# Performance work log

Hardware: AMD Instinct MI355X
Metric: run time of the kernel (lower is better)

The kernel has to match this reference:

```python
import jax, jax.numpy as jnp
import numpy as np

H, I, E, K = 1024, 2048, 8, 2
B, T = 4, 2048


def setup_inputs() -> dict:
    key = jax.random.key(0)
    k0, k1, k2, k3 = jax.random.split(key, 4)
    x = jax.random.normal(k0, (B, T, H), dtype=jnp.float32)
    Wg = jax.random.normal(k1, (E, H), dtype=jnp.float32) * 0.02   # gate: Linear(H->E), weight [E,H]
    W1 = jax.random.normal(k2, (E, I, H), dtype=jnp.float32) * 0.02  # per-expert fc1 weights [I,H]
    W2 = jax.random.normal(k3, (E, H, I), dtype=jnp.float32) * 0.02  # per-expert fc2 weights [H,I]
    return {"x": x, "Wg": Wg, "W1": W1, "W2": W2, "top_k": K}


def reference(x, Wg, W1, W2, top_k):
    b, t, h = x.shape
    xf = x.reshape(-1, h)                                  # [N,H], N=B*T
    gate_probs = jax.nn.softmax(xf @ Wg.T, axis=-1)        # [N,E]
    topk_vals, topk_idx = jax.lax.top_k(gate_probs, top_k) # [N,k]
    # Dense all-expert SiLU-MLP (faithful to the original dense MoE):
    hid = jax.nn.silu(jnp.einsum('nh,eih->nei', xf, W1))   # [N,E,I]
    all_outs = jnp.einsum('nei,ehi->neh', hid, W2)         # [N,E,H]
    topk_outs = jnp.take_along_axis(all_outs, topk_idx[:, :, None], axis=1)  # [N,k,H]
    weighted = (topk_outs * topk_vals[:, :, None]).sum(axis=1)               # [N,H]
    return weighted.reshape(b, t, h)
```

## Files before the change

### kernel.cpp

```cpp
#include <hip/hip_runtime.h>
#include <hip/hip_bf16.h>

#define HH 1024
#define II 2048
#define EE 8
#define NTOK 8192
#define NPAIR (NTOK * 2)

typedef __attribute__((ext_vector_type(8))) short bf16x8;
typedef __attribute__((ext_vector_type(4))) float f32x4;
typedef unsigned int u32;

__device__ __forceinline__ ushort f2bf(float f) {
    union { float f; unsigned u; } v; v.f = f;
    unsigned r = v.u + 0x7fffu + ((v.u >> 16) & 1u);
    return (ushort)(r >> 16);
}

__device__ __forceinline__ void gload16(const void* g, void* l) {
    __builtin_amdgcn_global_load_lds((const __attribute__((address_space(1))) u32*)g,
                                     (__attribute__((address_space(3))) u32*)l, 16, 0, 0);
}

__device__ __forceinline__ int expert_off(const int* __restrict__ counts, int e) {
    int off = 0;
#pragma unroll
    for (int i = 0; i < EE; i++) off += (i < e) ? counts[i] : 0;
    return off;
}

__global__ __launch_bounds__(256) void cvtw_kernel(
    const float* __restrict__ W1, const float* __restrict__ W2,
    ushort* __restrict__ W1b, ushort* __restrict__ W2b)
{
    const int N1 = EE * II * HH / 4;
    const int i = blockIdx.x * 256 + threadIdx.x;
    const float4 f = (i < N1) ? ((const float4*)W1)[i] : ((const float4*)W2)[i - N1];
    union { ushort h[4]; uint2 u; } pk;
    pk.h[0] = f2bf(f.x); pk.h[1] = f2bf(f.y); pk.h[2] = f2bf(f.z); pk.h[3] = f2bf(f.w);
    if (i < N1) ((uint2*)W1b)[i] = pk.u;
    else        ((uint2*)W2b)[i - N1] = pk.u;
}

__global__ __launch_bounds__(256) void gate_kernel(
    const float* __restrict__ x, const float* __restrict__ Wg,
    int* __restrict__ counts, int* __restrict__ tki, float* __restrict__ tkv,
    ushort* __restrict__ xb)
{
    __shared__ int hist[EE];
    const int tid = threadIdx.x;
    if (tid < EE) hist[tid] = 0;
    __syncthreads();

    const int w = tid >> 6, lane = tid & 63;

#pragma unroll 1
    for (int t = 0; t < 8; t++) {
        const int n = blockIdx.x * 32 + w * 8 + t;
        const float* xr = x + (size_t)n * HH;
        float4 xv[4];
#pragma unroll
        for (int c = 0; c < 4; c++) xv[c] = *(const float4*)(xr + c * 256 + lane * 4);

#pragma unroll
        for (int c = 0; c < 4; c++) {
            union { ushort h[4]; uint2 u; } pk;
            pk.h[0] = f2bf(xv[c].x); pk.h[1] = f2bf(xv[c].y);
            pk.h[2] = f2bf(xv[c].z); pk.h[3] = f2bf(xv[c].w);
            *(uint2*)(xb + (size_t)n * HH + c * 256 + lane * 4) = pk.u;
        }

        float dot[EE];
#pragma unroll
        for (int e = 0; e < EE; e++) {
            float s = 0.f;
#pragma unroll
            for (int c = 0; c < 4; c++) {
                const float4 wv = *(const float4*)(Wg + e * HH + c * 256 + lane * 4);
                s += xv[c].x * wv.x + xv[c].y * wv.y + xv[c].z * wv.z + xv[c].w * wv.w;
            }
            for (int off = 32; off > 0; off >>= 1) s += __shfl_down(s, off);
            dot[e] = s;
        }
        if (lane == 0) {
            float m = dot[0];
#pragma unroll
            for (int e = 1; e < EE; e++) m = fmaxf(m, dot[e]);
            float p[EE]; float sum = 0.f;
#pragma unroll
            for (int e = 0; e < EE; e++) { p[e] = __expf(dot[e] - m); sum += p[e]; }
            const float inv = 1.f / sum;
            int i0 = 0; float v0 = p[0];
#pragma unroll
            for (int e = 1; e < EE; e++) if (p[e] > v0) { v0 = p[e]; i0 = e; }
            int i1 = -1; float v1 = -1.f;
#pragma unroll
            for (int e = 0; e < EE; e++) if (e != i0 && p[e] > v1) { v1 = p[e]; i1 = e; }
            tki[n * 2 + 0] = i0; tkv[n * 2 + 0] = v0 * inv;
            tki[n * 2 + 1] = i1; tkv[n * 2 + 1] = v1 * inv;
            atomicAdd(&hist[i0], 1);
            atomicAdd(&hist[i1], 1);
        }
    }
    __syncthreads();
    if (tid < EE) atomicAdd(&counts[tid], hist[tid]);
}

__global__ __launch_bounds__(256) void scatter_kernel(
    const int* __restrict__ tki, const float* __restrict__ tkv,
    const int* __restrict__ counts,
    int* __restrict__ cursor, int* __restrict__ stok, float* __restrict__ sval)
{
    __shared__ int hist[EE];
    __shared__ int base[EE];
    const int tid = threadIdx.x;
    const int id = blockIdx.x * 256 + tid;
    if (tid < EE) hist[tid] = 0;
    __syncthreads();
    const int e = tki[id];
    const int loc = atomicAdd(&hist[e], 1);
    __syncthreads();
    if (tid < EE) {
        int off = 0;
        for (int i = 0; i < tid; i++) off += counts[i];
        base[tid] = off + atomicAdd(&cursor[tid], hist[tid]);
    }
    __syncthreads();
    const int p = base[e] + loc;
    stok[p] = id >> 1;
    sval[p] = tkv[id];
}

template <bool PRE>
__global__ __launch_bounds__(256) void fc1_kernel(
    const float* __restrict__ x, const ushort* __restrict__ xb,
    const float* __restrict__ W1, const ushort* __restrict__ W1b,
    const int* __restrict__ counts,
    const int* __restrict__ stok, ushort* __restrict__ hid)
{
    const int e = blockIdx.z;
    const int cnt = counts[e];
    const int row0 = blockIdx.y * 128;
    if (row0 >= cnt) return;
    const int off = expert_off(counts, e);
    const int col0 = blockIdx.x * 128;

    __shared__ __align__(16) ushort As[128 * 64];
    __shared__ __align__(16) ushort Bs[128 * 64];

    const int tid = threadIdx.x;
    const int w = tid >> 6, lane = tid & 63;
    const int quad = lane >> 4, l16 = lane & 15;
    const int wm = (w >> 1) * 64, wn = (w & 1) * 64;
    const int l7 = l16 & 7;

    f32x4 acc[4][4];
#pragma unroll
    for (int mi = 0; mi < 4; mi++)
#pragma unroll
        for (int ni = 0; ni < 4; ni++) acc[mi][ni] = f32x4{0.f, 0.f, 0.f, 0.f};

    const int sub = lane >> 3;
    const int chk = lane & 7;
    const int gchk = chk ^ sub;
    int tokA[4];
    const int fr = tid >> 1;
    const int fc = (tid & 1) * 32;
    int tokF = 0;
    if (PRE) {
#pragma unroll
        for (int i = 0; i < 4; i++) {
            int r = row0 + (w * 4 + i) * 8 + sub;
            if (r >= cnt) r = cnt - 1;
            tokA[i] = stok[off + r];
        }
    } else {
        int r = row0 + fr;
        if (r >= cnt) r = cnt - 1;
        tokF = stok[off + r];
    }

    if (PRE) {
#pragma unroll 1
        for (int it = 0; it < HH / 64; it++) {
            const int k0 = it * 64;
            __syncthreads();
#pragma unroll
            for (int i = 0; i < 4; i++) {
                const ushort* gA = xb + (size_t)tokA[i] * HH + k0 + gchk * 8;
                gload16(gA, &As[(w * 4 + i) * 512]);
                const ushort* gB = W1b + ((size_t)e * II + col0 + (w * 4 + i) * 8 + sub) * HH + k0 + gchk * 8;
                gload16(gB, &Bs[(w * 4 + i) * 512]);
            }
            __syncthreads();
#pragma unroll
            for (int kk = 0; kk < 2; kk++) {
                const int pos = ((kk * 4 + quad) ^ l7) * 8;
                bf16x8 af[4], bb[4];
#pragma unroll
                for (int mi = 0; mi < 4; mi++)
                    af[mi] = *(const bf16x8*)&As[(wm + mi * 16 + l16) * 64 + pos];
#pragma unroll
                for (int ni = 0; ni < 4; ni++)
                    bb[ni] = *(const bf16x8*)&Bs[(wn + ni * 16 + l16) * 64 + pos];
#pragma unroll
                for (int mi = 0; mi < 4; mi++)
#pragma unroll
                    for (int ni = 0; ni < 4; ni++)
                        acc[mi][ni] = __builtin_amdgcn_mfma_f32_16x16x32_bf16(af[mi], bb[ni], acc[mi][ni], 0, 0, 0);
            }
        }
    } else {
#pragma unroll 1
        for (int k0 = 0; k0 < HH; k0 += 64) {
            __syncthreads();
#pragma unroll
            for (int c = 0; c < 32; c += 4) {
                const int u = fc + c;
                const int sw = ((u >> 3) ^ (fr & 7)) * 8 + (u & 7);
                const float4 f = *(const float4*)(x + (size_t)tokF * HH + k0 + u);
                union { ushort h[4]; uint2 u2; } pk;
                pk.h[0] = f2bf(f.x); pk.h[1] = f2bf(f.y); pk.h[2] = f2bf(f.z); pk.h[3] = f2bf(f.w);
                *(uint2*)&As[fr * 64 + sw] = pk.u2;
                const float4 g = *(const float4*)(W1 + ((size_t)e * II + col0 + fr) * HH + k0 + u);
                pk.h[0] = f2bf(g.x); pk.h[1] = f2bf(g.y); pk.h[2] = f2bf(g.z); pk.h[3] = f2bf(g.w);
                *(uint2*)&Bs[fr * 64 + sw] = pk.u2;
            }
            __syncthreads();
#pragma unroll
            for (int kk = 0; kk < 2; kk++) {
                const int pos = ((kk * 4 + quad) ^ l7) * 8;
                bf16x8 af[4], bb[4];
#pragma unroll
                for (int mi = 0; mi < 4; mi++)
                    af[mi] = *(const bf16x8*)&As[(wm + mi * 16 + l16) * 64 + pos];
#pragma unroll
                for (int ni = 0; ni < 4; ni++)
                    bb[ni] = *(const bf16x8*)&Bs[(wn + ni * 16 + l16) * 64 + pos];
#pragma unroll
                for (int mi = 0; mi < 4; mi++)
#pragma unroll
                    for (int ni = 0; ni < 4; ni++)
                        acc[mi][ni] = __builtin_amdgcn_mfma_f32_16x16x32_bf16(af[mi], bb[ni], acc[mi][ni], 0, 0, 0);
            }
        }
    }

    const int cnt_rem = cnt - row0;
#pragma unroll
    for (int mi = 0; mi < 4; mi++) {
#pragma unroll
        for (int j = 0; j < 4; j++) {
            const int r = wm + mi * 16 + quad * 4 + j;
            if (r < cnt_rem) {
                ushort* hrow = hid + (size_t)(off + row0 + r) * II + col0 + wn + l16;
#pragma unroll
                for (int ni = 0; ni < 4; ni++) {
                    const float v = acc[mi][ni][j];
                    const float s = v / (1.f + __expf(-v));
                    hrow[ni * 16] = f2bf(s);
                }
            }
        }
    }
}

template <bool PRE>
__global__ __launch_bounds__(256) void fc2_kernel(
    const ushort* __restrict__ hid,
    const float* __restrict__ W2, const ushort* __restrict__ W2b,
    const int* __restrict__ counts,
    const int* __restrict__ stok, const float* __restrict__ sval,
    float* __restrict__ out)
{
    const int e = blockIdx.z;
    const int cnt = counts[e];
    const int row0 = blockIdx.y * 128;
    if (row0 >= cnt) return;
    const int off = expert_off(counts, e);
    const int col0 = blockIdx.x * 128;

    __shared__ __align__(16) ushort As[128 * 64];
    __shared__ __align__(16) ushort Bs[128 * 64];

    const int tid = threadIdx.x;
    const int w = tid >> 6, lane = tid & 63;
    const int quad = lane >> 4, l16 = lane & 15;
    const int wm = (w >> 1) * 64, wn = (w & 1) * 64;
    const int l7 = l16 & 7;

    f32x4 acc[4][4];
#pragma unroll
    for (int mi = 0; mi < 4; mi++)
#pragma unroll
        for (int ni = 0; ni < 4; ni++) acc[mi][ni] = f32x4{0.f, 0.f, 0.f, 0.f};

    const int sub = lane >> 3;
    const int chk = lane & 7;
    const int gchk = chk ^ sub;
    size_t slotA[4];
#pragma unroll
    for (int i = 0; i < 4; i++) {
        int s = off + row0 + (w * 4 + i) * 8 + sub;
        if (s > NPAIR - 1) s = NPAIR - 1;
        slotA[i] = (size_t)s;
    }
    const int fr = tid >> 1;
    const int fc = (tid & 1) * 32;

    if (PRE) {
#pragma unroll 1
        for (int it = 0; it < II / 64; it++) {
            const int k0 = it * 64;
            __syncthreads();
#pragma unroll
            for (int i = 0; i < 4; i++) {
                const ushort* gA = hid + slotA[i] * II + k0 + gchk * 8;
                gload16(gA, &As[(w * 4 + i) * 512]);
                const ushort* gB = W2b + ((size_t)e * HH + col0 + (w * 4 + i) * 8 + sub) * II + k0 + gchk * 8;
                gload16(gB, &Bs[(w * 4 + i) * 512]);
            }
            __syncthreads();
#pragma unroll
            for (int kk = 0; kk < 2; kk++) {
                const int pos = ((kk * 4 + quad) ^ l7) * 8;
                bf16x8 af[4], bb[4];
#pragma unroll
                for (int mi = 0; mi < 4; mi++)
                    af[mi] = *(const bf16x8*)&As[(wm + mi * 16 + l16) * 64 + pos];
#pragma unroll
                for (int ni = 0; ni < 4; ni++)
                    bb[ni] = *(const bf16x8*)&Bs[(wn + ni * 16 + l16) * 64 + pos];
#pragma unroll
                for (int mi = 0; mi < 4; mi++)
#pragma unroll
                    for (int ni = 0; ni < 4; ni++)
                        acc[mi][ni] = __builtin_amdgcn_mfma_f32_16x16x32_bf16(af[mi], bb[ni], acc[mi][ni], 0, 0, 0);
            }
        }
    } else {
#pragma unroll 1
        for (int k0 = 0; k0 < II; k0 += 64) {
            __syncthreads();
#pragma unroll
            for (int i = 0; i < 4; i++) {
                const ushort* gA = hid + slotA[i] * II + k0 + gchk * 8;
                gload16(gA, &As[(w * 4 + i) * 512]);
            }
#pragma unroll
            for (int c = 0; c < 32; c += 4) {
                const int u = fc + c;
                const int sw = ((u >> 3) ^ (fr & 7)) * 8 + (u & 7);
                const float4 g = *(const float4*)(W2 + ((size_t)e * HH + col0 + fr) * II + k0 + u);
                union { ushort h[4]; uint2 u2; } pk;
                pk.h[0] = f2bf(g.x); pk.h[1] = f2bf(g.y); pk.h[2] = f2bf(g.z); pk.h[3] = f2bf(g.w);
                *(uint2*)&Bs[fr * 64 + sw] = pk.u2;
            }
            __syncthreads();
#pragma unroll
            for (int kk = 0; kk < 2; kk++) {
                const int pos = ((kk * 4 + quad) ^ l7) * 8;
                bf16x8 af[4], bb[4];
#pragma unroll
                for (int mi = 0; mi < 4; mi++)
                    af[mi] = *(const bf16x8*)&As[(wm + mi * 16 + l16) * 64 + pos];
#pragma unroll
                for (int ni = 0; ni < 4; ni++)
                    bb[ni] = *(const bf16x8*)&Bs[(wn + ni * 16 + l16) * 64 + pos];
#pragma unroll
                for (int mi = 0; mi < 4; mi++)
#pragma unroll
                    for (int ni = 0; ni < 4; ni++)
                        acc[mi][ni] = __builtin_amdgcn_mfma_f32_16x16x32_bf16(af[mi], bb[ni], acc[mi][ni], 0, 0, 0);
            }
        }
    }

    const int cnt_rem = cnt - row0;
#pragma unroll
    for (int mi = 0; mi < 4; mi++) {
#pragma unroll
        for (int j = 0; j < 4; j++) {
            const int r = wm + mi * 16 + quad * 4 + j;
            if (r < cnt_rem) {
                const int p = off + row0 + r;
                const int token = stok[p];
                const float val = sval[p];
                float* orow = out + (size_t)token * HH + col0 + wn + l16;
#pragma unroll
                for (int ni = 0; ni < 4; ni++)
                    atomicAdd(&orow[ni * 16], val * acc[mi][ni][j]);
            }
        }
    }
}

extern "C" void kernel_launch(void* const* d_in, const int* in_sizes, int n_in,
                              void* d_out, int out_size, void* d_ws, size_t ws_size,
                              hipStream_t stream) {
    const float* x  = (const float*)d_in[0];
    const float* Wg = (const float*)d_in[1];
    const float* W1 = (const float*)d_in[2];
    const float* W2 = (const float*)d_in[3];
    float* out = (float*)d_out;

    char* wsb = (char*)d_ws;
    int*    counts = (int*)(wsb + 0);
    int*    cursor = (int*)(wsb + 64);
    int*    tki    = (int*)(wsb + 256);
    float*  tkv    = (float*)(wsb + 256 + 65536);
    int*    stok   = (int*)(wsb + 256 + 2 * 65536);
    float*  sval   = (float*)(wsb + 256 + 3 * 65536);
    ushort* hid    = (ushort*)(wsb + 262400);
    ushort* W1b    = (ushort*)(wsb + 262400 + 67108864ull);
    ushort* W2b    = (ushort*)(wsb + 262400 + 100663296ull);
    ushort* xb     = (ushort*)(wsb + 262400 + 134217728ull);
    const size_t REQ = 262400ull + 134217728ull + 16777216ull;
    const bool pre = ws_size >= REQ;

    hipMemsetAsync(wsb, 0, 256, stream);
    hipMemsetAsync(d_out, 0, (size_t)out_size * sizeof(float), stream);

    gate_kernel<<<NTOK / 32, 256, 0, stream>>>(x, Wg, counts, tki, tkv, xb);
    scatter_kernel<<<NPAIR / 256, 256, 0, stream>>>(tki, tkv, counts, cursor, stok, sval);

    if (pre) {
        cvtw_kernel<<<(2 * EE * II * HH / 4) / 256, 256, 0, stream>>>(W1, W2, W1b, W2b);
        fc1_kernel<true><<<dim3(II / 128, NPAIR / 128, EE), 256, 0, stream>>>(x, xb, W1, W1b, counts, stok, hid);
        fc2_kernel<true><<<dim3(HH / 128, NPAIR / 128, EE), 256, 0, stream>>>(hid, W2, W2b, counts, stok, hid == nullptr ? nullptr : sval, out);
    } else {
        fc1_kernel<false><<<dim3(II / 128, NPAIR / 128, EE), 256, 0, stream>>>(x, xb, W1, W1b, counts, stok, hid);
        fc2_kernel<false><<<dim3(HH / 128, NPAIR / 128, EE), 256, 0, stream>>>(hid, W2, W2b, counts, stok, sval, out);
    }
}
```

Before: 429.7 us.

## Replace fc2 atomic scatter-add with per-slot stores and a gather-combine kernel

fc2 now writes unweighted per-pair outputs into a sorted-slot temp buffer with plain stores instead of weighted atomicAdds into the output. A new gather kernel uses the pair-to-slot map that scatter now records, reads both expert rows for each token, applies the gate weights and writes the output directly. This also drops the output memset. It costs an extra 64MB temp round trip and one more kernel launch, and it only runs when the workspace is large enough.

```diff
diff --git a/kernel.cpp b/kernel.cpp
--- a/kernel.cpp
+++ b/kernel.cpp
@@ -109,7 +109,8 @@
 __global__ __launch_bounds__(256) void scatter_kernel(
     const int* __restrict__ tki, const float* __restrict__ tkv,
     const int* __restrict__ counts,
-    int* __restrict__ cursor, int* __restrict__ stok, float* __restrict__ sval)
+    int* __restrict__ cursor, int* __restrict__ stok, float* __restrict__ sval,
+    int* __restrict__ pslot)
 {
     __shared__ int hist[EE];
     __shared__ int base[EE];
@@ -129,6 +130,25 @@
     const int p = base[e] + loc;
     stok[p] = id >> 1;
     sval[p] = tkv[id];
+    pslot[id] = p;
+}
+
+__global__ __launch_bounds__(256) void gather_kernel(
+    const float* __restrict__ tmp, const float* __restrict__ tkv,
+    const int* __restrict__ pslot, float* __restrict__ out)
+{
+    const int t = blockIdx.x;
+    const int tid = threadIdx.x;
+    const int p0 = pslot[2 * t], p1 = pslot[2 * t + 1];
+    const float v0 = tkv[2 * t], v1 = tkv[2 * t + 1];
+    const float4 a = ((const float4*)(tmp + (size_t)p0 * HH))[tid];
+    const float4 b = ((const float4*)(tmp + (size_t)p1 * HH))[tid];
+    float4 o;
+    o.x = v0 * a.x + v1 * b.x;
+    o.y = v0 * a.y + v1 * b.y;
+    o.z = v0 * a.z + v1 * b.z;
+    o.w = v0 * a.w + v1 * b.w;
+    ((float4*)(out + (size_t)t * HH))[tid] = o;
 }
 
 template <bool PRE>
@@ -265,13 +285,13 @@
     }
 }
 
-template <bool PRE>
+template <bool PRE, bool TMP>
 __global__ __launch_bounds__(256) void fc2_kernel(
     const ushort* __restrict__ hid,
     const float* __restrict__ W2, const ushort* __restrict__ W2b,
     const int* __restrict__ counts,
     const int* __restrict__ stok, const float* __restrict__ sval,
-    float* __restrict__ out)
+    float* __restrict__ tmp, float* __restrict__ out)
 {
     const int e = blockIdx.z;
     const int cnt = counts[e];
@@ -384,12 +404,19 @@
             const int r = wm + mi * 16 + quad * 4 + j;
             if (r < cnt_rem) {
                 const int p = off + row0 + r;
-                const int token = stok[p];
-                const float val = sval[p];
-                float* orow = out + (size_t)token * HH + col0 + wn + l16;
-#pragma unroll
-                for (int ni = 0; ni < 4; ni++)
-                    atomicAdd(&orow[ni * 16], val * acc[mi][ni][j]);
+                if (TMP) {
+                    float* orow = tmp + (size_t)p * HH + col0 + wn + l16;
+#pragma unroll
+                    for (int ni = 0; ni < 4; ni++)
+                        orow[ni * 16] = acc[mi][ni][j];
+                } else {
+                    const int token = stok[p];
+                    const float val = sval[p];
+                    float* orow = out + (size_t)token * HH + col0 + wn + l16;
+#pragma unroll
+                    for (int ni = 0; ni < 4; ni++)
+                        atomicAdd(&orow[ni * 16], val * acc[mi][ni][j]);
+                }
             }
         }
     }
@@ -411,25 +438,36 @@
     float*  tkv    = (float*)(wsb + 256 + 65536);
     int*    stok   = (int*)(wsb + 256 + 2 * 65536);
     float*  sval   = (float*)(wsb + 256 + 3 * 65536);
-    ushort* hid    = (ushort*)(wsb + 262400);
-    ushort* W1b    = (ushort*)(wsb + 262400 + 67108864ull);
-    ushort* W2b    = (ushort*)(wsb + 262400 + 100663296ull);
-    ushort* xb     = (ushort*)(wsb + 262400 + 134217728ull);
-    const size_t REQ = 262400ull + 134217728ull + 16777216ull;
-    const bool pre = ws_size >= REQ;
+    int*    pslot  = (int*)(wsb + 256 + 4 * 65536);
+    const size_t HDR = 256 + 5 * 65536;
+    ushort* hid    = (ushort*)(wsb + HDR);
+    ushort* W1b    = (ushort*)(wsb + HDR + 67108864ull);
+    ushort* W2b    = (ushort*)(wsb + HDR + 100663296ull);
+    ushort* xb     = (ushort*)(wsb + HDR + 134217728ull);
+    float*  tmp    = (float*)(wsb + HDR + 150994944ull);
+    const size_t REQ1 = HDR + 150994944ull;
+    const size_t REQ2 = REQ1 + 67108864ull;
+    const bool pre  = ws_size >= REQ1;
+    const bool tmpp = ws_size >= REQ2;
 
     hipMemsetAsync(wsb, 0, 256, stream);
-    hipMemsetAsync(d_out, 0, (size_t)out_size * sizeof(float), stream);
+    if (!tmpp)
+        hipMemsetAsync(d_out, 0, (size_t)out_size * sizeof(float), stream);
 
     gate_kernel<<<NTOK / 32, 256, 0, stream>>>(x, Wg, counts, tki, tkv, xb);
-    scatter_kernel<<<NPAIR / 256, 256, 0, stream>>>(tki, tkv, counts, cursor, stok, sval);
+    scatter_kernel<<<NPAIR / 256, 256, 0, stream>>>(tki, tkv, counts, cursor, stok, sval, pslot);
 
     if (pre) {
         cvtw_kernel<<<(2 * EE * II * HH / 4) / 256, 256, 0, stream>>>(W1, W2, W1b, W2b);
         fc1_kernel<true><<<dim3(II / 128, NPAIR / 128, EE), 256, 0, stream>>>(x, xb, W1, W1b, counts, stok, hid);
-        fc2_kernel<true><<<dim3(HH / 128, NPAIR / 128, EE), 256, 0, stream>>>(hid, W2, W2b, counts, stok, hid == nullptr ? nullptr : sval, out);
+        if (tmpp) {
+            fc2_kernel<true, true><<<dim3(HH / 128, NPAIR / 128, EE), 256, 0, stream>>>(hid, W2, W2b, counts, stok, sval, tmp, out);
+            gather_kernel<<<NTOK, 256, 0, stream>>>(tmp, tkv, pslot, out);
+        } else {
+            fc2_kernel<true, false><<<dim3(HH / 128, NPAIR / 128, EE), 256, 0, stream>>>(hid, W2, W2b, counts, stok, sval, tmp, out);
+        }
     } else {
         fc1_kernel<false><<<dim3(II / 128, NPAIR / 128, EE), 256, 0, stream>>>(x, xb, W1, W1b, counts, stok, hid);
-        fc2_kernel<false><<<dim3(HH / 128, NPAIR / 128, EE), 256, 0, stream>>>(hid, W2, W2b, counts, stok, sval, out);
-    }
-}
+        fc2_kernel<false, false><<<dim3(HH / 128, NPAIR / 128, EE), 256, 0, stream>>>(hid, W2, W2b, counts, stok, sval, tmp, out);
+    }
+}
```

Measured after the change: 407.0 us. 1.06x faster.
